# Performance work log

Hardware: AMD Instinct MI355X
Metric: run time of the kernel (lower is better)

The kernel has to match this reference:

```python
import jax, jax.numpy as jnp
import numpy as np

H = 128          # input hidden dim
HID = 128        # expert hidden width
OUT = 128        # out_channels
NR = 8           # n_routed
NS = 2           # n_shared
RDIM = 16        # router feature dim


def setup_inputs() -> dict:
    key = jax.random.key(0)
    ks = jax.random.split(key, 11)
    s = 0.05
    x = jax.random.normal(ks[0], (2, 32, 32, 32, H), dtype=jnp.float32)
    # router params
    Wr1 = jax.random.normal(ks[1], (H, RDIM), dtype=jnp.float32) * s
    br1 = jnp.zeros((RDIM,), dtype=jnp.float32)
    Wr2 = jax.random.normal(ks[2], (RDIM, NR), dtype=jnp.float32) * s
    br2 = jnp.zeros((NR,), dtype=jnp.float32)
    # routed expert params, stacked on leading expert axis
    We1 = jax.random.normal(ks[3], (NR, H, HID), dtype=jnp.float32) * s
    be1 = jnp.zeros((NR, HID), dtype=jnp.float32)
    We2 = jax.random.normal(ks[4], (NR, HID, OUT), dtype=jnp.float32) * s
    be2 = jnp.zeros((NR, OUT), dtype=jnp.float32)
    # shared expert params
    Ws1 = jax.random.normal(ks[5], (NS, H, HID), dtype=jnp.float32) * s
    bs1 = jnp.zeros((NS, HID), dtype=jnp.float32)
    Ws2 = jax.random.normal(ks[6], (NS, HID, OUT), dtype=jnp.float32) * s
    bs2 = jnp.zeros((NS, OUT), dtype=jnp.float32)
    return dict(x=x, Wr1=Wr1, br1=br1, Wr2=Wr2, br2=br2,
                We1=We1, be1=be1, We2=We2, be2=be2,
                Ws1=Ws1, bs1=bs1, Ws2=Ws2, bs2=bs2)


def reference(x, Wr1, br1, Wr2, br2, We1, be1, We2, be2, Ws1, bs1, Ws2, bs2):
    # router: Dense(16) -> relu -> Dense(n_routed) -> softmax
    rf = jax.nn.relu(jnp.einsum('...h,hr->...r', x, Wr1) + br1)
    logits = jnp.einsum('...r,re->...e', rf, Wr2) + br2
    gate = jax.nn.softmax(logits, axis=-1)                      # [..., NR]
    threshold = 1.0 / NR
    mask = (gate > threshold).astype(gate.dtype)
    mg = gate * mask
    mg = mg / (jnp.sum(mg, axis=-1, keepdims=True) + 1e-8)
    # routed experts (batched over expert axis e): Dense -> gelu(tanh) -> Dense
    hr = jax.nn.gelu(jnp.einsum('...h,ehd->...ed', x, We1) + be1)   # [..., NR, HID]
    ro = jnp.einsum('...ed,edo->...eo', hr, We2) + be2              # [..., NR, OUT]
    routed_agg = jnp.einsum('...eo,...e->...o', ro, mg)
    # shared experts summed
    hs = jax.nn.gelu(jnp.einsum('...h,ehd->...ed', x, Ws1) + bs1)   # [..., NS, HID]
    so = jnp.einsum('...ed,edo->...eo', hs, Ws2) + bs2              # [..., NS, OUT]
    shared_agg = jnp.sum(so, axis=-2)
    return routed_agg + shared_agg
```

## Files before the change

kernel.cpp:

```cpp
#include <hip/hip_runtime.h>
#include <hip/hip_bf16.h>

typedef __bf16 bf16x8 __attribute__((ext_vector_type(8)));
typedef float  f32x16 __attribute__((ext_vector_type(16)));
typedef float  f32x4  __attribute__((ext_vector_type(4)));
typedef float  f32x2  __attribute__((ext_vector_type(2)));

static __device__ __forceinline__ f32x16 mfma32(bf16x8 a, bf16x8 b, f32x16 c) {
    return __builtin_amdgcn_mfma_f32_32x32x16_bf16(a, b, c, 0, 0, 0);
}

static __device__ __forceinline__ void gl_lds16(const void* g, void* l) {
    __builtin_amdgcn_global_load_lds(
        (const __attribute__((address_space(1))) unsigned int*)g,
        (__attribute__((address_space(3))) unsigned int*)l,
        16, 0, 0);
}

#define GELU_C1 2.30220820f
#define GELU_C2 0.10294324f

static __device__ __forceinline__ bf16x8 gelu8(f32x16 a, int base, float gv) {
    bf16x8 r;
    #pragma unroll
    for (int p = 0; p < 4; ++p) {
        f32x2 hh; hh[0] = a[base + 2 * p]; hh[1] = a[base + 2 * p + 1];
        f32x2 tt = hh * hh;
        f32x2 pp;
        pp[0] = fmaf(tt[0], -GELU_C2, -GELU_C1);
        pp[1] = fmaf(tt[1], -GELU_C2, -GELU_C1);
        f32x2 mm = hh * pp;
        float e0 = __builtin_amdgcn_exp2f(mm[0]);
        float e1 = __builtin_amdgcn_exp2f(mm[1]);
        float q0 = __builtin_amdgcn_rcpf(1.f + e0);
        float q1 = __builtin_amdgcn_rcpf(1.f + e1);
        r[2 * p]     = (__bf16)(hh[0] * q0 * gv);
        r[2 * p + 1] = (__bf16)(hh[1] * q1 * gv);
    }
    return r;
}

__global__ __launch_bounds__(256) void pack_kernel(
    const float* __restrict__ We1, const float* __restrict__ be1,
    const float* __restrict__ Ws1, const float* __restrict__ bs1,
    const float* __restrict__ We2, const float* __restrict__ Ws2,
    const float* __restrict__ Wr1, const float* __restrict__ br1,
    const float* __restrict__ Wr2, const float* __restrict__ br2,
    __bf16* __restrict__ w1p, __bf16* __restrict__ w2p,
    float* __restrict__ be1p,
    double* __restrict__ wr1d, double* __restrict__ br1d,
    double* __restrict__ wr2d, double* __restrict__ br2d)
{
    int tid = blockIdx.x * 256 + threadIdx.x;
    if (tid < 20480) {
        int l  = tid & 63;
        int ks = (tid >> 6) & 7;
        int nt = (tid >> 9) & 3;
        int e  = tid >> 11;
        const float* src = (e < 8) ? (We1 + e * 16384) : (Ws1 + (e - 8) * 16384);
        int n  = nt * 32 + (l & 31);
        int kb = ks * 16 + (l >> 5) * 8;
        bf16x8 v;
        #pragma unroll
        for (int j = 0; j < 8; ++j) v[j] = (__bf16)src[(kb + j) * 128 + n];
        *(bf16x8*)(w1p + (size_t)tid * 8) = v;
    } else if (tid < 40960) {
        int t2 = tid - 20480;
        int l  = t2 & 63;
        int ot = (t2 >> 6) & 3;
        int kq = (t2 >> 8) & 7;
        int e  = t2 >> 11;
        const float* src = (e < 8) ? (We2 + e * 16384) : (Ws2 + (e - 8) * 16384);
        int o  = 32 * ot + (l & 31);
        int lh = l >> 5;
        bf16x8 v;
        #pragma unroll
        for (int j = 0; j < 8; ++j) {
            int hid = 16 * kq + 8 * (j >> 2) + 4 * lh + (j & 3);
            v[j] = (__bf16)src[hid * 128 + o];
        }
        *(bf16x8*)(w2p + (size_t)t2 * 8) = v;
    } else if (tid < 42240) {
        int i  = tid - 40960;
        int r  = i & 15;
        int h2 = (i >> 4) & 1;
        int nt = (i >> 5) & 3;
        int e  = i >> 7;
        int n  = 32 * nt + (r & 3) + 8 * (r >> 2) + 4 * h2;
        be1p[i] = (e < 8) ? be1[e * 128 + n] : bs1[(e - 8) * 128 + n];
    } else if (tid < 44288) {
        int i = tid - 42240;
        wr1d[i] = (double)Wr1[i];
    } else if (tid < 44416) {
        int i = tid - 44288;
        wr2d[i] = (double)Wr2[i];
    } else if (tid < 44432) {
        int i = tid - 44416;
        br1d[i] = (double)br1[i];
    } else if (tid < 44440) {
        int i = tid - 44432;
        br2d[i] = (double)br2[i];
    }
}

__global__ __launch_bounds__(256) void router_kernel(
    const float* __restrict__ x,
    const double* __restrict__ wr1d, const double* __restrict__ br1d,
    const double* __restrict__ wr2d, const double* __restrict__ br2d,
    float* __restrict__ gates)
{
    __shared__ __align__(16) char lds[41472];
    float*  xs  = (float*)lds;
    double* rfs = (double*)(lds + 33280);

    const int t    = threadIdx.x;
    const int tok0 = blockIdx.x * 64;

    #pragma unroll
    for (int i = 0; i < 8; ++i) {
        int cid = i * 256 + t;
        int m = cid >> 5;
        int c = cid & 31;
        f32x4 v = *(const f32x4*)(x + (size_t)(tok0 + m) * 128 + c * 4);
        f32x2 s0, s1;
        s0[0] = v[0]; s0[1] = v[1]; s1[0] = v[2]; s1[1] = v[3];
        *(f32x2*)(xs + m * 130 + c * 4)     = s0;
        *(f32x2*)(xs + m * 130 + c * 4 + 2) = s1;
    }
    __syncthreads();

    {
        const int tok = t & 63;
        const int rq  = (t >> 6) * 4;
        const int rqs = __builtin_amdgcn_readfirstlane(rq);
        double rf4[4];
        #pragma unroll
        for (int j = 0; j < 4; ++j) rf4[j] = br1d[rqs + j];
        const float* xr = xs + tok * 130;
        #pragma unroll 4
        for (int c = 0; c < 64; ++c) {
            f32x2 xv2 = *(const f32x2*)(xr + c * 2);
            #pragma unroll
            for (int q = 0; q < 2; ++q) {
                double xv = (double)xv2[q];
                int k = c * 2 + q;
                #pragma unroll
                for (int j = 0; j < 4; ++j)
                    rf4[j] = fma(xv, wr1d[k * 16 + rqs + j], rf4[j]);
            }
        }
        #pragma unroll
        for (int j = 0; j < 4; ++j)
            rfs[tok * 16 + rq + j] = rf4[j] > 0.0 ? rf4[j] : 0.0;
    }
    __syncthreads();

    if (t < 64) {
        double lg[8];
        #pragma unroll
        for (int j = 0; j < 8; ++j) lg[j] = br2d[j];
        #pragma unroll
        for (int r = 0; r < 16; ++r) {
            double rv = rfs[t * 16 + r];
            #pragma unroll
            for (int j = 0; j < 8; ++j)
                lg[j] = fma(rv, wr2d[r * 8 + j], lg[j]);
        }
        double mx = lg[0];
        #pragma unroll
        for (int j = 1; j < 8; ++j) mx = lg[j] > mx ? lg[j] : mx;
        double ex[8]; double s = 0.0;
        #pragma unroll
        for (int j = 0; j < 8; ++j) { ex[j] = exp(lg[j] - mx); s += ex[j]; }
        double ms = 0.0;
        bool mk[8];
        #pragma unroll
        for (int j = 0; j < 8; ++j) {
            mk[j] = (8.0 * ex[j] > s);
            ms += mk[j] ? ex[j] : 0.0;
        }
        double inv = 1.0 / (ms + s * 1e-8);
        f32x4 o0, o1;
        #pragma unroll
        for (int j = 0; j < 4; ++j) {
            o0[j] = mk[j]     ? (float)(ex[j] * inv)     : 0.f;
            o1[j] = mk[4 + j] ? (float)(ex[4 + j] * inv) : 0.f;
        }
        *(f32x4*)(gates + (size_t)(tok0 + t) * 8)     = o0;
        *(f32x4*)(gates + (size_t)(tok0 + t) * 8 + 4) = o1;
    }
}

#define GEMM2_STEP(W)                                   \
    acc0 = mfma32(h0, W[0], acc0);                      \
    acc1 = mfma32(h0, W[1], acc1);                      \
    acc2 = mfma32(h0, W[2], acc2);                      \
    acc3 = mfma32(h0, W[3], acc3);                      \
    acc0 = mfma32(h1, W[4], acc0);                      \
    acc1 = mfma32(h1, W[5], acc1);                      \
    acc2 = mfma32(h1, W[6], acc2);                      \
    acc3 = mfma32(h1, W[7], acc3);

__global__ __launch_bounds__(256, 2) void moe_main_kernel(
    const float* __restrict__ x, const float* __restrict__ gates,
    const __bf16* __restrict__ w1p, const __bf16* __restrict__ w2p,
    const float* __restrict__ be1p,
    const float* __restrict__ be2, const float* __restrict__ bs2,
    float* __restrict__ out)
{
    __shared__ __align__(16) char lds[65536];

    const int t    = threadIdx.x;
    const int lane = t & 63;
    const int wv   = t >> 6;
    const int l31  = lane & 31;
    const int hi   = lane >> 5;
    const int tok0 = blockIdx.x * 128;
    const size_t row = (size_t)(tok0 + 32 * wv + l31);

    #define FILL_EXPERT(e)                                                      \
    {                                                                           \
        const char* g1 = (const char*)(w1p + (size_t)(e) * 16384)               \
                         + wv * 8192 + lane * 16;                               \
        const char* g2 = (const char*)(w2p + (size_t)(e) * 16384)               \
                         + wv * 8192 + lane * 16;                               \
        char* l1 = lds + wv * 8192;                                             \
        char* l2 = lds + 32768 + wv * 8192;                                     \
        _Pragma("unroll")                                                       \
        for (int i = 0; i < 8; ++i) {                                           \
            gl_lds16(g1 + i * 1024, l1 + i * 1024);                             \
            gl_lds16(g2 + i * 1024, l2 + i * 1024);                             \
        }                                                                       \
    }

    FILL_EXPERT(0)

    bf16x8 xf[8];
    {
        const float* xr = x + row * 128 + 8 * hi;
        #pragma unroll
        for (int ks = 0; ks < 8; ++ks) {
            f32x4 va = *(const f32x4*)(xr + 16 * ks);
            f32x4 vb = *(const f32x4*)(xr + 16 * ks + 4);
            bf16x8 v;
            v[0]=(__bf16)va[0]; v[1]=(__bf16)va[1]; v[2]=(__bf16)va[2]; v[3]=(__bf16)va[3];
            v[4]=(__bf16)vb[0]; v[5]=(__bf16)vb[1]; v[6]=(__bf16)vb[2]; v[7]=(__bf16)vb[3];
            xf[ks] = v;
        }
    }

    f32x16 acc0, acc1, acc2, acc3;
    #pragma unroll
    for (int i = 0; i < 16; ++i) { acc0[i]=0.f; acc1[i]=0.f; acc2[i]=0.f; acc3[i]=0.f; }

    const bf16x8* W1L = (const bf16x8*)(lds);
    const bf16x8* W2L = (const bf16x8*)(lds + 32768);

    asm volatile("s_waitcnt vmcnt(0)" ::: "memory");
    __builtin_amdgcn_s_barrier();
    __builtin_amdgcn_sched_barrier(0);

    #pragma unroll 1
    for (int e = 0; e < 10; ++e) {
        float gv = 1.0f;
        if (e < 8) gv = gates[row * 8 + e];

        bf16x8 wb[8];
        #pragma unroll
        for (int ks = 0; ks < 8; ++ks) wb[ks] = W1L[ks * 64 + lane];

        #pragma unroll
        for (int nt = 0; nt < 4; ++nt) {
            bf16x8 wB[8];
            #pragma unroll
            for (int f = 0; f < 8; ++f) wB[f] = W2L[(8 * nt + f) * 64 + lane];

            const f32x16 bfr = *(const f32x16*)(be1p + ((e * 4 + nt) * 2 + hi) * 16);

            __builtin_amdgcn_s_setprio(1);
            f32x16 alo = bfr;
            f32x16 ahi;
            #pragma unroll
            for (int i = 0; i < 16; ++i) ahi[i] = 0.f;
            #pragma unroll
            for (int ks = 0; ks < 4; ++ks) {
                alo = mfma32(wb[ks],     xf[ks],     alo);
                ahi = mfma32(wb[ks + 4], xf[ks + 4], ahi);
            }
            __builtin_amdgcn_s_setprio(0);

            if (nt < 3) {
                #pragma unroll
                for (int ks = 0; ks < 8; ++ks)
                    wb[ks] = W1L[((nt + 1) * 8 + ks) * 64 + lane];
            }

            f32x16 a = alo + ahi;
            bf16x8 h0 = gelu8(a, 0, gv);
            bf16x8 h1 = gelu8(a, 8, gv);

            __builtin_amdgcn_s_setprio(1);
            GEMM2_STEP(wB)
            __builtin_amdgcn_s_setprio(0);
        }

        __builtin_amdgcn_s_barrier();
        __builtin_amdgcn_sched_barrier(0);
        if (e < 9) {
            FILL_EXPERT(e + 1)
            asm volatile("s_waitcnt vmcnt(0)" ::: "memory");
            __builtin_amdgcn_s_barrier();
            __builtin_amdgcn_sched_barrier(0);
        }
    }

    {
        float be2c[4][8], bsc[4];
        #pragma unroll
        for (int ot = 0; ot < 4; ++ot) {
            int o = 32 * ot + l31;
            bsc[ot] = bs2[o] + bs2[128 + o];
            #pragma unroll
            for (int ee = 0; ee < 8; ++ee) be2c[ot][ee] = be2[ee * 128 + o];
        }
        #pragma unroll
        for (int r = 0; r < 16; ++r) {
            int mrow = (r & 3) + 8 * (r >> 2) + 4 * hi;
            size_t trow = (size_t)(tok0 + 32 * wv + mrow);
            f32x4 g0 = *(const f32x4*)(gates + trow * 8);
            f32x4 g1 = *(const f32x4*)(gates + trow * 8 + 4);
            size_t obase = trow * 128 + l31;
            #pragma unroll
            for (int ot = 0; ot < 4; ++ot) {
                float b = bsc[ot];
                #pragma unroll
                for (int ee = 0; ee < 4; ++ee) b = fmaf(g0[ee], be2c[ot][ee], b);
                #pragma unroll
                for (int ee = 0; ee < 4; ++ee) b = fmaf(g1[ee], be2c[ot][4 + ee], b);
                float av = (ot == 0) ? acc0[r] : (ot == 1) ? acc1[r]
                         : (ot == 2) ? acc2[r] : acc3[r];
                out[obase + 32 * ot] = av + b;
            }
        }
    }
    #undef FILL_EXPERT
}

extern "C" void kernel_launch(void* const* d_in, const int* in_sizes, int n_in,
                              void* d_out, int out_size, void* d_ws, size_t ws_size,
                              hipStream_t stream)
{
    const float* x   = (const float*)d_in[0];
    const float* Wr1 = (const float*)d_in[1];
    const float* br1 = (const float*)d_in[2];
    const float* Wr2 = (const float*)d_in[3];
    const float* br2 = (const float*)d_in[4];
    const float* We1 = (const float*)d_in[5];
    const float* be1 = (const float*)d_in[6];
    const float* We2 = (const float*)d_in[7];
    const float* be2 = (const float*)d_in[8];
    const float* Ws1 = (const float*)d_in[9];
    const float* bs1 = (const float*)d_in[10];
    const float* Ws2 = (const float*)d_in[11];
    const float* bs2 = (const float*)d_in[12];

    __bf16* w1p  = (__bf16*)d_ws;
    __bf16* w2p  = (__bf16*)((char*)d_ws + 327680);
    float*  be1p = (float*)((char*)d_ws + 655360);
    double* wr1d = (double*)((char*)d_ws + 660480);
    double* wr2d = (double*)((char*)d_ws + 676864);
    double* br1d = (double*)((char*)d_ws + 677888);
    double* br2d = (double*)((char*)d_ws + 678016);
    float*  gts  = (float*)((char*)d_ws + 720896);

    pack_kernel<<<174, 256, 0, stream>>>(We1, be1, Ws1, bs1, We2, Ws2,
                                         Wr1, br1, Wr2, br2,
                                         w1p, w2p, be1p, wr1d, br1d, wr2d, br2d);
    router_kernel<<<1024, 256, 0, stream>>>(x, wr1d, br1d, wr2d, br2d, gts);
    moe_main_kernel<<<512, 256, 0, stream>>>(x, gts, w1p, w2p, be1p, be2, bs2,
                                             (float*)d_out);
}
```

Baseline: 185.4 us.

## Process two 32-token tiles per wave and overlap next expert weight fill

```diff
diff --git a/kernel.cpp b/kernel.cpp
--- a/kernel.cpp
+++ b/kernel.cpp
@@ -191,17 +191,17 @@
     }
 }
 
-#define GEMM2_STEP(W)                                   \
-    acc0 = mfma32(h0, W[0], acc0);                      \
-    acc1 = mfma32(h0, W[1], acc1);                      \
-    acc2 = mfma32(h0, W[2], acc2);                      \
-    acc3 = mfma32(h0, W[3], acc3);                      \
-    acc0 = mfma32(h1, W[4], acc0);                      \
-    acc1 = mfma32(h1, W[5], acc1);                      \
-    acc2 = mfma32(h1, W[6], acc2);                      \
-    acc3 = mfma32(h1, W[7], acc3);
-
-__global__ __launch_bounds__(256, 2) void moe_main_kernel(
+#define GEMM2_STEP(ACC, W)                              \
+    ACC##0 = mfma32(h0, W[0], ACC##0);                  \
+    ACC##1 = mfma32(h0, W[1], ACC##1);                  \
+    ACC##2 = mfma32(h0, W[2], ACC##2);                  \
+    ACC##3 = mfma32(h0, W[3], ACC##3);                  \
+    ACC##0 = mfma32(h1, W[4], ACC##0);                  \
+    ACC##1 = mfma32(h1, W[5], ACC##1);                  \
+    ACC##2 = mfma32(h1, W[6], ACC##2);                  \
+    ACC##3 = mfma32(h1, W[7], ACC##3);
+
+__global__ __launch_bounds__(256, 1) void moe_main_kernel(
     const float* __restrict__ x, const float* __restrict__ gates,
     const __bf16* __restrict__ w1p, const __bf16* __restrict__ w2p,
     const float* __restrict__ be1p,
@@ -215,8 +215,9 @@
     const int wv   = t >> 6;
     const int l31  = lane & 31;
     const int hi   = lane >> 5;
-    const int tok0 = blockIdx.x * 128;
-    const size_t row = (size_t)(tok0 + 32 * wv + l31);
+    const int tok0 = blockIdx.x * 256;
+    const size_t rowA = (size_t)(tok0 + 64 * wv + l31);
+    const size_t rowB = rowA + 32;
 
     #define FILL_EXPERT(e)                                                      \
     {                                                                           \
@@ -235,23 +236,33 @@
 
     FILL_EXPERT(0)
 
-    bf16x8 xf[8];
+    bf16x8 xfA[8], xfB[8];
     {
-        const float* xr = x + row * 128 + 8 * hi;
+        const float* xrA = x + rowA * 128 + 8 * hi;
+        const float* xrB = x + rowB * 128 + 8 * hi;
         #pragma unroll
         for (int ks = 0; ks < 8; ++ks) {
-            f32x4 va = *(const f32x4*)(xr + 16 * ks);
-            f32x4 vb = *(const f32x4*)(xr + 16 * ks + 4);
+            f32x4 va = *(const f32x4*)(xrA + 16 * ks);
+            f32x4 vb = *(const f32x4*)(xrA + 16 * ks + 4);
             bf16x8 v;
             v[0]=(__bf16)va[0]; v[1]=(__bf16)va[1]; v[2]=(__bf16)va[2]; v[3]=(__bf16)va[3];
             v[4]=(__bf16)vb[0]; v[5]=(__bf16)vb[1]; v[6]=(__bf16)vb[2]; v[7]=(__bf16)vb[3];
-            xf[ks] = v;
-        }
-    }
-
-    f32x16 acc0, acc1, acc2, acc3;
+            xfA[ks] = v;
+            f32x4 wa = *(const f32x4*)(xrB + 16 * ks);
+            f32x4 wb_ = *(const f32x4*)(xrB + 16 * ks + 4);
+            bf16x8 u;
+            u[0]=(__bf16)wa[0]; u[1]=(__bf16)wa[1]; u[2]=(__bf16)wa[2]; u[3]=(__bf16)wa[3];
+            u[4]=(__bf16)wb_[0]; u[5]=(__bf16)wb_[1]; u[6]=(__bf16)wb_[2]; u[7]=(__bf16)wb_[3];
+            xfB[ks] = u;
+        }
+    }
+
+    f32x16 accA0, accA1, accA2, accA3, accB0, accB1, accB2, accB3;
     #pragma unroll
-    for (int i = 0; i < 16; ++i) { acc0[i]=0.f; acc1[i]=0.f; acc2[i]=0.f; acc3[i]=0.f; }
+    for (int i = 0; i < 16; ++i) {
+        accA0[i]=0.f; accA1[i]=0.f; accA2[i]=0.f; accA3[i]=0.f;
+        accB0[i]=0.f; accB1[i]=0.f; accB2[i]=0.f; accB3[i]=0.f;
+    }
 
     const bf16x8* W1L = (const bf16x8*)(lds);
     const bf16x8* W2L = (const bf16x8*)(lds + 32768);
@@ -260,14 +271,14 @@
     __builtin_amdgcn_s_barrier();
     __builtin_amdgcn_sched_barrier(0);
 
+    bf16x8 wb[8];
+    #pragma unroll
+    for (int ks = 0; ks < 8; ++ks) wb[ks] = W1L[ks * 64 + lane];
+
     #pragma unroll 1
     for (int e = 0; e < 10; ++e) {
-        float gv = 1.0f;
-        if (e < 8) gv = gates[row * 8 + e];
-
-        bf16x8 wb[8];
-        #pragma unroll
-        for (int ks = 0; ks < 8; ++ks) wb[ks] = W1L[ks * 64 + lane];
+        float gvA = 1.0f, gvB = 1.0f;
+        if (e < 8) { gvA = gates[rowA * 8 + e]; gvB = gates[rowB * 8 + e]; }
 
         #pragma unroll
         for (int nt = 0; nt < 4; ++nt) {
@@ -277,17 +288,17 @@
 
             const f32x16 bfr = *(const f32x16*)(be1p + ((e * 4 + nt) * 2 + hi) * 16);
 
-            __builtin_amdgcn_s_setprio(1);
-            f32x16 alo = bfr;
-            f32x16 ahi;
-            #pragma unroll
-            for (int i = 0; i < 16; ++i) ahi[i] = 0.f;
+            f32x16 aloA = bfr, aloB = bfr;
+            f32x16 ahiA, ahiB;
+            #pragma unroll
+            for (int i = 0; i < 16; ++i) { ahiA[i] = 0.f; ahiB[i] = 0.f; }
             #pragma unroll
             for (int ks = 0; ks < 4; ++ks) {
-                alo = mfma32(wb[ks],     xf[ks],     alo);
-                ahi = mfma32(wb[ks + 4], xf[ks + 4], ahi);
-            }
-            __builtin_amdgcn_s_setprio(0);
+                aloA = mfma32(wb[ks],     xfA[ks],     aloA);
+                ahiA = mfma32(wb[ks + 4], xfA[ks + 4], ahiA);
+                aloB = mfma32(wb[ks],     xfB[ks],     aloB);
+                ahiB = mfma32(wb[ks + 4], xfB[ks + 4], ahiB);
+            }
 
             if (nt < 3) {
                 #pragma unroll
@@ -295,22 +306,33 @@
                     wb[ks] = W1L[((nt + 1) * 8 + ks) * 64 + lane];
             }
 
-            f32x16 a = alo + ahi;
-            bf16x8 h0 = gelu8(a, 0, gv);
-            bf16x8 h1 = gelu8(a, 8, gv);
-
-            __builtin_amdgcn_s_setprio(1);
-            GEMM2_STEP(wB)
-            __builtin_amdgcn_s_setprio(0);
-        }
-
-        __builtin_amdgcn_s_barrier();
-        __builtin_amdgcn_sched_barrier(0);
+            if (nt == 3) {
+                asm volatile("s_waitcnt lgkmcnt(0)" ::: "memory");
+                __builtin_amdgcn_s_barrier();
+                __builtin_amdgcn_sched_barrier(0);
+                if (e < 9) FILL_EXPERT(e + 1)
+            }
+
+            {
+                f32x16 a = aloA + ahiA;
+                bf16x8 h0 = gelu8(a, 0, gvA);
+                bf16x8 h1 = gelu8(a, 8, gvA);
+                GEMM2_STEP(accA, wB)
+            }
+            {
+                f32x16 a = aloB + ahiB;
+                bf16x8 h0 = gelu8(a, 0, gvB);
+                bf16x8 h1 = gelu8(a, 8, gvB);
+                GEMM2_STEP(accB, wB)
+            }
+        }
+
         if (e < 9) {
-            FILL_EXPERT(e + 1)
             asm volatile("s_waitcnt vmcnt(0)" ::: "memory");
             __builtin_amdgcn_s_barrier();
             __builtin_amdgcn_sched_barrier(0);
+            #pragma unroll
+            for (int ks = 0; ks < 8; ++ks) wb[ks] = W1L[ks * 64 + lane];
         }
     }
 
@@ -324,22 +346,30 @@
             for (int ee = 0; ee < 8; ++ee) be2c[ot][ee] = be2[ee * 128 + o];
         }
         #pragma unroll
-        for (int r = 0; r < 16; ++r) {
-            int mrow = (r & 3) + 8 * (r >> 2) + 4 * hi;
-            size_t trow = (size_t)(tok0 + 32 * wv + mrow);
-            f32x4 g0 = *(const f32x4*)(gates + trow * 8);
-            f32x4 g1 = *(const f32x4*)(gates + trow * 8 + 4);
-            size_t obase = trow * 128 + l31;
-            #pragma unroll
-            for (int ot = 0; ot < 4; ++ot) {
-                float b = bsc[ot];
+        for (int mi = 0; mi < 2; ++mi) {
+            #pragma unroll
+            for (int r = 0; r < 16; ++r) {
+                int mrow = (r & 3) + 8 * (r >> 2) + 4 * hi;
+                size_t trow = (size_t)(tok0 + 64 * wv + 32 * mi + mrow);
+                f32x4 g0 = *(const f32x4*)(gates + trow * 8);
+                f32x4 g1 = *(const f32x4*)(gates + trow * 8 + 4);
+                size_t obase = trow * 128 + l31;
                 #pragma unroll
-                for (int ee = 0; ee < 4; ++ee) b = fmaf(g0[ee], be2c[ot][ee], b);
-                #pragma unroll
-                for (int ee = 0; ee < 4; ++ee) b = fmaf(g1[ee], be2c[ot][4 + ee], b);
-                float av = (ot == 0) ? acc0[r] : (ot == 1) ? acc1[r]
-                         : (ot == 2) ? acc2[r] : acc3[r];
-                out[obase + 32 * ot] = av + b;
+                for (int ot = 0; ot < 4; ++ot) {
+                    float b = bsc[ot];
+                    #pragma unroll
+                    for (int ee = 0; ee < 4; ++ee) b = fmaf(g0[ee], be2c[ot][ee], b);
+                    #pragma unroll
+                    for (int ee = 0; ee < 4; ++ee) b = fmaf(g1[ee], be2c[ot][4 + ee], b);
+                    float av;
+                    if (mi == 0)
+                        av = (ot == 0) ? accA0[r] : (ot == 1) ? accA1[r]
+                           : (ot == 2) ? accA2[r] : accA3[r];
+                    else
+                        av = (ot == 0) ? accB0[r] : (ot == 1) ? accB1[r]
+                           : (ot == 2) ? accB2[r] : accB3[r];
+                    out[obase + 32 * ot] = av + b;
+                }
             }
         }
     }
@@ -377,6 +407,6 @@
                                          Wr1, br1, Wr2, br2,
                                          w1p, w2p, be1p, wr1d, br1d, wr2d, br2d);
     router_kernel<<<1024, 256, 0, stream>>>(x, wr1d, br1d, wr2d, br2d, gts);
-    moe_main_kernel<<<512, 256, 0, stream>>>(x, gts, w1p, w2p, be1p, be2, bs2,
+    moe_main_kernel<<<256, 256, 0, stream>>>(x, gts, w1p, w2p, be1p, be2, bs2,
                                              (float*)d_out);
 }
```

After: 187.1 us. Within noise of the previous version (+0.9%).

## Split W1/W2 LDS fills to overlap weight loads with GEMM phases

Applied to the files above, without the earlier changes.

```diff
diff --git a/kernel.cpp b/kernel.cpp
--- a/kernel.cpp
+++ b/kernel.cpp
@@ -20,22 +20,27 @@
 #define GELU_C1 2.30220820f
 #define GELU_C2 0.10294324f
 
-static __device__ __forceinline__ bf16x8 gelu8(f32x16 a, int base, float gv) {
+static __device__ __forceinline__ bf16x8 gelu8p(f32x16 a, int base, f32x2 gv2) {
+    const f32x2 c2  = {-GELU_C2, -GELU_C2};
+    const f32x2 c1  = {-GELU_C1, -GELU_C1};
+    const f32x2 one = {1.f, 1.f};
     bf16x8 r;
     #pragma unroll
     for (int p = 0; p < 4; ++p) {
         f32x2 hh; hh[0] = a[base + 2 * p]; hh[1] = a[base + 2 * p + 1];
         f32x2 tt = hh * hh;
-        f32x2 pp;
-        pp[0] = fmaf(tt[0], -GELU_C2, -GELU_C1);
-        pp[1] = fmaf(tt[1], -GELU_C2, -GELU_C1);
+        f32x2 pp = tt * c2 + c1;
         f32x2 mm = hh * pp;
-        float e0 = __builtin_amdgcn_exp2f(mm[0]);
-        float e1 = __builtin_amdgcn_exp2f(mm[1]);
-        float q0 = __builtin_amdgcn_rcpf(1.f + e0);
-        float q1 = __builtin_amdgcn_rcpf(1.f + e1);
-        r[2 * p]     = (__bf16)(hh[0] * q0 * gv);
-        r[2 * p + 1] = (__bf16)(hh[1] * q1 * gv);
+        f32x2 ee;
+        ee[0] = __builtin_amdgcn_exp2f(mm[0]);
+        ee[1] = __builtin_amdgcn_exp2f(mm[1]);
+        f32x2 dd = one + ee;
+        f32x2 qq;
+        qq[0] = __builtin_amdgcn_rcpf(dd[0]);
+        qq[1] = __builtin_amdgcn_rcpf(dd[1]);
+        f32x2 gg = (hh * qq) * gv2;
+        r[2 * p]     = (__bf16)gg[0];
+        r[2 * p + 1] = (__bf16)gg[1];
     }
     return r;
 }
@@ -191,16 +196,6 @@
     }
 }
 
-#define GEMM2_STEP(W)                                   \
-    acc0 = mfma32(h0, W[0], acc0);                      \
-    acc1 = mfma32(h0, W[1], acc1);                      \
-    acc2 = mfma32(h0, W[2], acc2);                      \
-    acc3 = mfma32(h0, W[3], acc3);                      \
-    acc0 = mfma32(h1, W[4], acc0);                      \
-    acc1 = mfma32(h1, W[5], acc1);                      \
-    acc2 = mfma32(h1, W[6], acc2);                      \
-    acc3 = mfma32(h1, W[7], acc3);
-
 __global__ __launch_bounds__(256, 2) void moe_main_kernel(
     const float* __restrict__ x, const float* __restrict__ gates,
     const __bf16* __restrict__ w1p, const __bf16* __restrict__ w2p,
@@ -218,22 +213,16 @@
     const int tok0 = blockIdx.x * 128;
     const size_t row = (size_t)(tok0 + 32 * wv + l31);
 
-    #define FILL_EXPERT(e)                                                      \
+    #define FILL32K(dst, src)                                                   \
     {                                                                           \
-        const char* g1 = (const char*)(w1p + (size_t)(e) * 16384)               \
-                         + wv * 8192 + lane * 16;                               \
-        const char* g2 = (const char*)(w2p + (size_t)(e) * 16384)               \
-                         + wv * 8192 + lane * 16;                               \
-        char* l1 = lds + wv * 8192;                                             \
-        char* l2 = lds + 32768 + wv * 8192;                                     \
+        const char* g_ = (const char*)(src) + wv * 8192 + lane * 16;            \
+        char* l_ = (dst) + wv * 8192;                                           \
         _Pragma("unroll")                                                       \
-        for (int i = 0; i < 8; ++i) {                                           \
-            gl_lds16(g1 + i * 1024, l1 + i * 1024);                             \
-            gl_lds16(g2 + i * 1024, l2 + i * 1024);                             \
-        }                                                                       \
-    }
-
-    FILL_EXPERT(0)
+        for (int i_ = 0; i_ < 8; ++i_)                                          \
+            gl_lds16(g_ + i_ * 1024, l_ + i_ * 1024);                           \
+    }
+
+    FILL32K(lds, w1p)
 
     bf16x8 xf[8];
     {
@@ -262,18 +251,18 @@
 
     #pragma unroll 1
     for (int e = 0; e < 10; ++e) {
+        FILL32K(lds + 32768, (const char*)w2p + (size_t)e * 32768)
+
         float gv = 1.0f;
         if (e < 8) gv = gates[row * 8 + e];
-
-        bf16x8 wb[8];
-        #pragma unroll
-        for (int ks = 0; ks < 8; ++ks) wb[ks] = W1L[ks * 64 + lane];
-
+        f32x2 gv2; gv2[0] = gv; gv2[1] = gv;
+
+        bf16x8 h[8];
         #pragma unroll
         for (int nt = 0; nt < 4; ++nt) {
-            bf16x8 wB[8];
-            #pragma unroll
-            for (int f = 0; f < 8; ++f) wB[f] = W2L[(8 * nt + f) * 64 + lane];
+            bf16x8 wb[8];
+            #pragma unroll
+            for (int ks = 0; ks < 8; ++ks) wb[ks] = W1L[(nt * 8 + ks) * 64 + lane];
 
             const f32x16 bfr = *(const f32x16*)(be1p + ((e * 4 + nt) * 2 + hi) * 16);
 
@@ -289,29 +278,33 @@
             }
             __builtin_amdgcn_s_setprio(0);
 
-            if (nt < 3) {
-                #pragma unroll
-                for (int ks = 0; ks < 8; ++ks)
-                    wb[ks] = W1L[((nt + 1) * 8 + ks) * 64 + lane];
-            }
-
             f32x16 a = alo + ahi;
-            bf16x8 h0 = gelu8(a, 0, gv);
-            bf16x8 h1 = gelu8(a, 8, gv);
-
-            __builtin_amdgcn_s_setprio(1);
-            GEMM2_STEP(wB)
-            __builtin_amdgcn_s_setprio(0);
-        }
-
+            h[2 * nt]     = gelu8p(a, 0, gv2);
+            h[2 * nt + 1] = gelu8p(a, 8, gv2);
+        }
+        asm volatile("s_waitcnt vmcnt(0)" ::: "memory");
         __builtin_amdgcn_s_barrier();
         __builtin_amdgcn_sched_barrier(0);
-        if (e < 9) {
-            FILL_EXPERT(e + 1)
-            asm volatile("s_waitcnt vmcnt(0)" ::: "memory");
-            __builtin_amdgcn_s_barrier();
-            __builtin_amdgcn_sched_barrier(0);
-        }
+
+        if (e < 9) FILL32K(lds, (const char*)w1p + (size_t)(e + 1) * 32768)
+
+        __builtin_amdgcn_s_setprio(1);
+        #pragma unroll
+        for (int kq = 0; kq < 8; ++kq) {
+            bf16x8 wB0 = W2L[(kq * 4 + 0) * 64 + lane];
+            bf16x8 wB1 = W2L[(kq * 4 + 1) * 64 + lane];
+            bf16x8 wB2 = W2L[(kq * 4 + 2) * 64 + lane];
+            bf16x8 wB3 = W2L[(kq * 4 + 3) * 64 + lane];
+            acc0 = mfma32(h[kq], wB0, acc0);
+            acc1 = mfma32(h[kq], wB1, acc1);
+            acc2 = mfma32(h[kq], wB2, acc2);
+            acc3 = mfma32(h[kq], wB3, acc3);
+        }
+        __builtin_amdgcn_s_setprio(0);
+
+        asm volatile("s_waitcnt vmcnt(0)" ::: "memory");
+        __builtin_amdgcn_s_barrier();
+        __builtin_amdgcn_sched_barrier(0);
     }
 
     {
@@ -343,7 +336,7 @@
             }
         }
     }
-    #undef FILL_EXPERT
+    #undef FILL32K
 }
 
 extern "C" void kernel_launch(void* const* d_in, const int* in_sizes, int n_in,
```

Result: slower. 193.8 us (+4.6%).
